# Kernel optimization log

Hardware: AMD Instinct MI355X
Metric: run time of the kernel (lower is better)

## Reference

```python
import jax, jax.numpy as jnp
import numpy as np

B, N, F = 256, 32, 256
NUM_PASSING = 2


def _fc_edges(n):
    # all ordered pairs (send -> rec), i != j, matching NRI-style encode matrices
    send, rec = [], []
    for i in range(n):
        for j in range(n):
            if i != j:
                send.append(i)
                rec.append(j)
    return np.array(send, np.int32), np.array(rec, np.int32)


def setup_inputs() -> dict:
    key = jax.random.key(0)
    ks = jax.random.split(key, 16)
    send_np, rec_np = _fc_edges(N)

    def xavier(k, shape):
        fan_in, fan_out = shape
        std = (2.0 / (fan_in + fan_out)) ** 0.5
        return jax.random.normal(k, shape, jnp.float32) * std

    bias = lambda d: jnp.full((d,), 0.1, jnp.float32)
    return {
        "x": jax.random.normal(ks[0], (B, N, F), jnp.float32),
        "rec_idx": jnp.asarray(rec_np),
        "send_idx": jnp.asarray(send_np),
        "w_in1": xavier(ks[1], (F, 256)), "b_in1": bias(256),
        "w_in2": xavier(ks[2], (256, 256)), "b_in2": bias(256),
        "w_e1": xavier(ks[3], (512, 256)), "b_e1": bias(256),
        "w_e2": xavier(ks[4], (256, 256)), "b_e2": bias(256),
        "w_n1": xavier(ks[5], (256, 256)), "b_n1": bias(256),
        "w_n2": xavier(ks[6], (256, 256)), "b_n2": bias(256),
    }


def _mlp(h, wa, ba, wb, bb):
    # Linear -> ReLU -> (Dropout p=0) -> Linear -> ReLU
    return jax.nn.relu(jax.nn.relu(h @ wa + ba) @ wb + bb)


def reference(x, rec_idx, send_idx,
              w_in1, b_in1, w_in2, b_in2,
              w_e1, b_e1, w_e2, b_e2,
              w_n1, b_n1, w_n2, b_n2):
    n_nodes = x.shape[-2]
    # in-degree per node == rec_encode.sum(0)
    deg = jax.ops.segment_sum(jnp.ones_like(rec_idx, x.dtype), rec_idx,
                              num_segments=n_nodes)  # [N]
    h = _mlp(x, w_in1, b_in1, w_in2, b_in2)  # [B, N, 256]
    for _ in range(NUM_PASSING):
        # node2edge: gather (== one-hot matmul), cat [sends, recs]
        edges = jnp.concatenate([h[:, send_idx, :], h[:, rec_idx, :]], axis=-1)  # [B, E, 512]
        e = _mlp(edges, w_e1, b_e1, w_e2, b_e2)  # [B, E, 256]
        # edge2node: scatter-sum by receiver then divide by in-degree (mean)
        e_t = jnp.swapaxes(e, 0, 1)  # [E, B, 256]
        agg = jax.ops.segment_sum(e_t, rec_idx, num_segments=n_nodes)  # [N, B, 256]
        agg = jnp.swapaxes(agg, 0, 1) / deg[None, :, None]  # [B, N, 256]
        h = _mlp(agg, w_n1, b_n1, w_n2, b_n2)
    return h
```

## Files before the change

kernel.cpp:

```cpp
#include <hip/hip_runtime.h>


typedef short bf16x8 __attribute__((ext_vector_type(8)));
typedef float f32x4 __attribute__((ext_vector_type(4)));
typedef unsigned short ushort_t;

__device__ __forceinline__ unsigned short f2bf(float f) {
    unsigned u = __float_as_uint(f);
    u += 0x7fff + ((u >> 16) & 1);
    return (unsigned short)(u >> 16);
}
__device__ __forceinline__ float lo16f(unsigned w) { return __uint_as_float(w << 16); }
__device__ __forceinline__ float hi16f(unsigned w) { return __uint_as_float(w & 0xffff0000u); }
__device__ __forceinline__ unsigned cvt_pk_bf16(float lo, float hi) {
    unsigned r;
    asm volatile("v_cvt_pk_bf16_f32 %0, %1, %2" : "=v"(r) : "v"(lo), "v"(hi));
    return r;
}
__device__ __forceinline__ void gload16(const void* g, void* l) {
    __builtin_amdgcn_global_load_lds(
        (const __attribute__((address_space(1))) void*)g,
        (__attribute__((address_space(3))) void*)l, 16, 0, 0);
}

__global__ __launch_bounds__(256) void prep_weights(
    const float* __restrict__ w_in1, const float* __restrict__ w_in2,
    const float* __restrict__ w_e1,  const float* __restrict__ w_e2,
    const float* __restrict__ w_n1,  const float* __restrict__ w_n2,
    ushort_t* __restrict__ dst)
{
    __shared__ ushort_t tile[32][264];
    const int wid = blockIdx.x >> 3;
    const int kb  = blockIdx.x & 7;
    const float* src;
    switch (wid) {
        case 0: src = w_in1; break;
        case 1: src = w_in2; break;
        case 2: src = w_e1; break;
        case 3: src = w_e1 + 65536; break;
        case 4: src = w_e2; break;
        case 5: src = w_n1; break;
        default: src = w_n2; break;
    }
    const int t = threadIdx.x;
#pragma unroll
    for (int k0 = 0; k0 < 32; k0++)
        tile[k0][t] = f2bf(src[(size_t)(kb * 32 + k0) * 256 + t]);
    __syncthreads();
    ushort_t* base = dst + wid * 65536 + kb * 8192 + t * 32;
    const int sw = (t >> 1) & 3;
#pragma unroll
    for (int kc = 0; kc < 4; kc++) {
        union { uint4 q; ushort_t u[8]; } w;
#pragma unroll
        for (int ko = 0; ko < 8; ko++) w.u[ko] = tile[kc * 8 + ko][t];
        *(uint4*)&base[(kc ^ sw) * 8] = w.q;
    }
}

__global__ __launch_bounds__(256) void conv_x(
    const float* __restrict__ x, ushort_t* __restrict__ xb, int n8)
{
    int i = blockIdx.x * 256 + threadIdx.x;
    if (i >= n8) return;
    const float4* p = (const float4*)x + (size_t)i * 2;
    float4 a = p[0], b = p[1];
    ushort4 o0 = make_ushort4(f2bf(a.x), f2bf(a.y), f2bf(a.z), f2bf(a.w));
    ushort4 o1 = make_ushort4(f2bf(b.x), f2bf(b.y), f2bf(b.z), f2bf(b.w));
    ((ushort4*)xb)[(size_t)i * 2]     = o0;
    ((ushort4*)xb)[(size_t)i * 2 + 1] = o1;
}


__device__ __forceinline__ void layer_to_lds(
    const ushort_t* __restrict__ wimg, const float* __restrict__ bias,
    const ushort_t* __restrict__ As, ushort_t* __restrict__ Ad,
    const int w, const int lr, const int lg)
{
    int boffs[4]; float4 b4[4];
#pragma unroll
    for (int fn = 0; fn < 4; fn++) {
        const int n = w * 64 + fn * 16 + lr;
        boffs[fn] = n * 32 + ((lg ^ ((n >> 1) & 3)) * 8);
        b4[fn] = *(const float4*)&bias[w * 64 + fn * 16 + lg * 4];
    }
    bf16x8 bc[4];
#pragma unroll
    for (int fn = 0; fn < 4; fn++) bc[fn] = *(const bf16x8*)&wimg[boffs[fn]];
    f32x4 acc[4][2] = {};
#pragma unroll
    for (int kb = 0; kb < 8; kb++) {
        bf16x8 bn[4];
        if (kb < 7)
#pragma unroll
            for (int fn = 0; fn < 4; fn++)
                bn[fn] = *(const bf16x8*)&wimg[(kb + 1) * 8192 + boffs[fn]];
        bf16x8 af[2];
#pragma unroll
        for (int fm = 0; fm < 2; fm++) {
            const int r = fm * 16 + lr;
            af[fm] = *(const bf16x8*)&As[r * 256 + (((kb * 4 + lg) ^ (r & 7)) * 8)];
        }
#pragma unroll
        for (int fn = 0; fn < 4; fn++)
#pragma unroll
            for (int fm = 0; fm < 2; fm++)
                acc[fn][fm] = __builtin_amdgcn_mfma_f32_16x16x32_bf16(
                    bc[fn], af[fm], acc[fn][fm], 0, 0, 0);
        if (kb < 7)
#pragma unroll
            for (int fn = 0; fn < 4; fn++) bc[fn] = bn[fn];
    }
#pragma unroll
    for (int fn = 0; fn < 4; fn++) {
        const int k0 = w * 64 + fn * 16 + lg * 4;
        const int kc = k0 >> 3, kj = k0 & 7;
#pragma unroll
        for (int fm = 0; fm < 2; fm++) {
            const int m = fm * 16 + lr;
            float v0 = fmaxf(acc[fn][fm][0] + b4[fn].x, 0.f);
            float v1 = fmaxf(acc[fn][fm][1] + b4[fn].y, 0.f);
            float v2 = fmaxf(acc[fn][fm][2] + b4[fn].z, 0.f);
            float v3 = fmaxf(acc[fn][fm][3] + b4[fn].w, 0.f);
            uint2 q = { cvt_pk_bf16(v0, v1), cvt_pk_bf16(v2, v3) };
            *(uint2*)&Ad[m * 256 + ((kc ^ (m & 7)) * 8) + kj] = q;
        }
    }
}

__device__ __forceinline__ void layer_e1(
    const ushort_t* __restrict__ wE, const float* __restrict__ bE,
    const ushort_t* __restrict__ As, ushort_t* __restrict__ UVb,
    const int m0, const int w, const int lr, const int lg)
{
    const ushort_t* wimg = (w < 2) ? wE : (wE + 65536);
    const int nb = (w & 1) * 128;
    int boffs[8]; float4 b4[8];
#pragma unroll
    for (int fn = 0; fn < 8; fn++) {
        const int n = nb + fn * 16 + lr;
        boffs[fn] = n * 32 + ((lg ^ ((n >> 1) & 3)) * 8);
        if (w < 2) b4[fn] = *(const float4*)&bE[nb + fn * 16 + lg * 4];
        else       b4[fn] = make_float4(0.f, 0.f, 0.f, 0.f);
    }
    bf16x8 bc[8];
#pragma unroll
    for (int fn = 0; fn < 8; fn++) bc[fn] = *(const bf16x8*)&wimg[boffs[fn]];
    f32x4 acc[8][2] = {};
#pragma unroll
    for (int kb = 0; kb < 8; kb++) {
        bf16x8 bn[8];
        if (kb < 7)
#pragma unroll
            for (int fn = 0; fn < 8; fn++)
                bn[fn] = *(const bf16x8*)&wimg[(kb + 1) * 8192 + boffs[fn]];
        bf16x8 af[2];
#pragma unroll
        for (int fm = 0; fm < 2; fm++) {
            const int r = fm * 16 + lr;
            af[fm] = *(const bf16x8*)&As[r * 256 + (((kb * 4 + lg) ^ (r & 7)) * 8)];
        }
#pragma unroll
        for (int fn = 0; fn < 8; fn++)
#pragma unroll
            for (int fm = 0; fm < 2; fm++)
                acc[fn][fm] = __builtin_amdgcn_mfma_f32_16x16x32_bf16(
                    bc[fn], af[fm], acc[fn][fm], 0, 0, 0);
        if (kb < 7)
#pragma unroll
            for (int fn = 0; fn < 8; fn++) bc[fn] = bn[fn];
    }
#pragma unroll
    for (int fn = 0; fn < 8; fn++) {
        const int nglob = w * 128 + fn * 16 + lg * 4;
#pragma unroll
        for (int fm = 0; fm < 2; fm++) {
            const int node = m0 + fm * 16 + lr;
            float v0 = acc[fn][fm][0] + b4[fn].x;
            float v1 = acc[fn][fm][1] + b4[fn].y;
            float v2 = acc[fn][fm][2] + b4[fn].z;
            float v3 = acc[fn][fm][3] + b4[fn].w;
            uint2 q = { cvt_pk_bf16(v0, v1), cvt_pk_bf16(v2, v3) };
            *(uint2*)&UVb[(size_t)node * 512 + nglob] = q;
        }
    }
}

__device__ __forceinline__ void layer_fin(
    const ushort_t* __restrict__ wimg, const float* __restrict__ bias,
    const ushort_t* __restrict__ As, float* __restrict__ out,
    const int m0, const int w, const int lr, const int lg)
{
    int boffs[4]; float4 b4[4];
#pragma unroll
    for (int fn = 0; fn < 4; fn++) {
        const int n = w * 64 + fn * 16 + lr;
        boffs[fn] = n * 32 + ((lg ^ ((n >> 1) & 3)) * 8);
        b4[fn] = *(const float4*)&bias[w * 64 + fn * 16 + lg * 4];
    }
    bf16x8 bc[4];
#pragma unroll
    for (int fn = 0; fn < 4; fn++) bc[fn] = *(const bf16x8*)&wimg[boffs[fn]];
    f32x4 acc[4][2] = {};
#pragma unroll
    for (int kb = 0; kb < 8; kb++) {
        bf16x8 bn[4];
        if (kb < 7)
#pragma unroll
            for (int fn = 0; fn < 4; fn++)
                bn[fn] = *(const bf16x8*)&wimg[(kb + 1) * 8192 + boffs[fn]];
        bf16x8 af[2];
#pragma unroll
        for (int fm = 0; fm < 2; fm++) {
            const int r = fm * 16 + lr;
            af[fm] = *(const bf16x8*)&As[r * 256 + (((kb * 4 + lg) ^ (r & 7)) * 8)];
        }
#pragma unroll
        for (int fn = 0; fn < 4; fn++)
#pragma unroll
            for (int fm = 0; fm < 2; fm++)
                acc[fn][fm] = __builtin_amdgcn_mfma_f32_16x16x32_bf16(
                    bc[fn], af[fm], acc[fn][fm], 0, 0, 0);
        if (kb < 7)
#pragma unroll
            for (int fn = 0; fn < 4; fn++) bc[fn] = bn[fn];
    }
#pragma unroll
    for (int fn = 0; fn < 4; fn++) {
        const int col = w * 64 + fn * 16 + lg * 4;
#pragma unroll
        for (int fm = 0; fm < 2; fm++) {
            const int row = m0 + fm * 16 + lr;
            float4 o;
            o.x = fmaxf(acc[fn][fm][0] + b4[fn].x, 0.f);
            o.y = fmaxf(acc[fn][fm][1] + b4[fn].y, 0.f);
            o.z = fmaxf(acc[fn][fm][2] + b4[fn].z, 0.f);
            o.w = fmaxf(acc[fn][fm][3] + b4[fn].w, 0.f);
            *(float4*)&out[(size_t)row * 256 + col] = o;
        }
    }
}

template <int THREE>
__global__ __launch_bounds__(256, 2) void mlp_chain(
    const ushort_t* __restrict__ in,
    const ushort_t* __restrict__ wA, const float* __restrict__ bA,
    const ushort_t* __restrict__ wB, const float* __restrict__ bB,
    const ushort_t* __restrict__ wE, const float* __restrict__ bE,
    void* __restrict__ out)
{
    __shared__ ushort_t A0[32 * 256];
    __shared__ ushort_t A1[32 * 256];
    const int m0 = blockIdx.x * 32;
    const int t = threadIdx.x;
    const int lane = t & 63, w = t >> 6;
    const int lr = lane & 15, lg = lane >> 4;

#pragma unroll
    for (int i = 0; i < 4; i++) {
        const int r = i * 8 + (t >> 5);
        const int p = t & 31;
        gload16(in + (size_t)(m0 + r) * 256 + ((p ^ (r & 7)) * 8), &A0[i * 2048 + t * 8]);
    }
    __syncthreads();

    layer_to_lds(wA, bA, A0, A1, w, lr, lg);
    __syncthreads();
    if constexpr (THREE) {
        layer_to_lds(wB, bB, A1, A0, w, lr, lg);
        __syncthreads();
        layer_e1(wE, bE, A0, (ushort_t*)out, m0, w, lr, lg);
    } else {
        layer_fin(wB, bB, A1, (float*)out, m0, w, lr, lg);
    }
}

__global__ __launch_bounds__(256, 2) void edge_fused(
    const ushort_t* __restrict__ UVb,
    const ushort_t* __restrict__ WBsw,
    const float* __restrict__ b2,
    ushort_t* __restrict__ agg)
{
    __shared__ ushort_t As[2][128 * 64];

    const int logical = (blockIdx.x & 7) * 256 + (blockIdx.x >> 3);
    const int bb = logical >> 3;
    const int g0 = (logical & 7) * 4;
    const int t = threadIdx.x;
    const int lane = t & 63;
    const int w = t >> 6;
    const int lr = lane & 15, lg = lane >> 4;

    const int brow = t >> 1;
    const int kh = t & 1;
    const int jr = brow >> 5;
    const int s = brow & 31;
    const int j = g0 + jr;
    const int si = (s == 31) ? j : (s + (s >= j ? 1 : 0));
    const ushort_t* up = UVb + (size_t)(bb * 32 + si) * 512 + kh * 32;
    const ushort_t* vp = UVb + (size_t)(bb * 32 + j) * 512 + 256 + kh * 32;
    const int rs7 = brow & 7;
    int aw[4];
#pragma unroll
    for (int i = 0; i < 4; i++)
        aw[i] = brow * 64 + (((kh * 4 + i) ^ rs7) * 8);

    const int acof0 = ((lg ^ (lr & 7)) * 8) + lr * 64;
    const int bbase = (w * 64 + lr) * 32 + ((lg ^ ((lr >> 1) & 3)) * 8);

    auto build = [&](int buf, const uint4* u, const uint4* v) {
#pragma unroll
        for (int i = 0; i < 4; i++) {
            uint4 q;
            q.x = cvt_pk_bf16(fmaxf(lo16f(u[i].x) + lo16f(v[i].x), 0.f),
                              fmaxf(hi16f(u[i].x) + hi16f(v[i].x), 0.f));
            q.y = cvt_pk_bf16(fmaxf(lo16f(u[i].y) + lo16f(v[i].y), 0.f),
                              fmaxf(hi16f(u[i].y) + hi16f(v[i].y), 0.f));
            q.z = cvt_pk_bf16(fmaxf(lo16f(u[i].z) + lo16f(v[i].z), 0.f),
                              fmaxf(hi16f(u[i].z) + hi16f(v[i].z), 0.f));
            q.w = cvt_pk_bf16(fmaxf(lo16f(u[i].w) + lo16f(v[i].w), 0.f),
                              fmaxf(hi16f(u[i].w) + hi16f(v[i].w), 0.f));
            *(uint4*)&As[buf][aw[i]] = q;
        }
    };

    {
        uint4 u[4], v[4];
#pragma unroll
        for (int i = 0; i < 4; i++) {
            u[i] = *(const uint4*)(up + i * 8);
            v[i] = *(const uint4*)(vp + i * 8);
        }
        build(0, u, v);
    }
    bf16x8 bc[2][4];
#pragma unroll
    for (int ks = 0; ks < 2; ks++)
#pragma unroll
        for (int fn = 0; fn < 4; fn++)
            bc[ks][fn] = *(const bf16x8*)&WBsw[ks * 8192 + bbase + fn * 512];

    f32x4 acc[8][4] = {};

#pragma unroll
    for (int kb = 0; kb < 4; kb++) {
        __syncthreads();
        uint4 u[4], v[4];
        if (kb < 3) {
            const ushort_t* upn = up + (kb + 1) * 64;
            const ushort_t* vpn = vp + (kb + 1) * 64;
#pragma unroll
            for (int i = 0; i < 4; i++) {
                u[i] = *(const uint4*)(upn + i * 8);
                v[i] = *(const uint4*)(vpn + i * 8);
            }
        }
        __builtin_amdgcn_s_setprio(1);
#pragma unroll
        for (int ks = 0; ks < 2; ks++) {
            bf16x8 af[8];
#pragma unroll
            for (int m = 0; m < 8; m++)
                af[m] = *(const bf16x8*)&As[kb & 1][m * 1024 + (acof0 ^ (ks * 32))];
#pragma unroll
            for (int fn = 0; fn < 4; fn++)
#pragma unroll
                for (int m = 0; m < 8; m++)
                    acc[m][fn] = __builtin_amdgcn_mfma_f32_16x16x32_bf16(
                        af[m], bc[ks][fn], acc[m][fn], 0, 0, 0);
        }
        __builtin_amdgcn_s_setprio(0);
        if (kb < 3) {
#pragma unroll
            for (int ks = 0; ks < 2; ks++)
#pragma unroll
                for (int fn = 0; fn < 4; fn++)
                    bc[ks][fn] = *(const bf16x8*)&WBsw[((kb + 1) * 2 + ks) * 8192
                                                       + bbase + fn * 512];
            build((kb + 1) & 1, u, v);
        }
    }

#pragma unroll
    for (int fn = 0; fn < 4; fn++) {
        const int col = w * 64 + fn * 16 + lr;
        const float bvf = b2[col];
#pragma unroll
        for (int recv = 0; recv < 4; recv++) {
            float sum = 0.f;
#pragma unroll
            for (int q = 0; q < 2; q++) {
                const int fm = recv * 2 + q;
#pragma unroll
                for (int r = 0; r < 4; r++) {
                    float v = fmaxf(acc[fm][fn][r] + bvf, 0.f);
                    if (!(q == 1 && lg == 3 && r == 3)) sum += v;
                }
            }
            sum += __shfl_xor(sum, 16);
            sum += __shfl_xor(sum, 32);
            if (lane < 16)
                agg[(size_t)(bb * 32 + g0 + recv) * 256 + col] = f2bf(sum * (1.0f / 31.0f));
        }
    }
}

extern "C" void kernel_launch(void* const* d_in, const int* in_sizes, int n_in,
                              void* d_out, int out_size, void* d_ws, size_t ws_size,
                              hipStream_t stream)
{
    const float* x     = (const float*)d_in[0];
    const float* w_in1 = (const float*)d_in[3];
    const float* b_in1 = (const float*)d_in[4];
    const float* w_in2 = (const float*)d_in[5];
    const float* b_in2 = (const float*)d_in[6];
    const float* w_e1  = (const float*)d_in[7];
    const float* b_e1  = (const float*)d_in[8];
    const float* w_e2  = (const float*)d_in[9];
    const float* b_e2  = (const float*)d_in[10];
    const float* w_n1  = (const float*)d_in[11];
    const float* b_n1  = (const float*)d_in[12];
    const float* w_n2  = (const float*)d_in[13];
    const float* b_n2  = (const float*)d_in[14];

    char* ws = (char*)d_ws;
    size_t off = 0;
    auto alloc = [&](size_t n) { char* p = ws + off; off += (n + 255) & ~(size_t)255; return p; };

    ushort_t* wt  = (ushort_t*)alloc(7 * 65536 * sizeof(ushort_t));
    ushort_t* xb  = (ushort_t*)alloc(8192 * 256 * 2);
    ushort_t* UVb = (ushort_t*)alloc(8192 * 512 * 2);
    ushort_t* ag  = (ushort_t*)alloc(8192 * 256 * 2);
    (void)ws_size; (void)in_sizes; (void)n_in; (void)out_size;

    prep_weights<<<56, 256, 0, stream>>>(w_in1, w_in2, w_e1, w_e2, w_n1, w_n2, wt);
    conv_x<<<1024, 256, 0, stream>>>(x, xb, 262144);

    mlp_chain<1><<<256, 256, 0, stream>>>(xb,
        wt + 0 * 65536, b_in1, wt + 1 * 65536, b_in2, wt + 2 * 65536, b_e1, UVb);
    edge_fused<<<2048, 256, 0, stream>>>(UVb, wt + 4 * 65536, b_e2, ag);
    mlp_chain<1><<<256, 256, 0, stream>>>(ag,
        wt + 5 * 65536, b_n1, wt + 6 * 65536, b_n2, wt + 2 * 65536, b_e1, UVb);
    edge_fused<<<2048, 256, 0, stream>>>(UVb, wt + 4 * 65536, b_e2, ag);
    mlp_chain<0><<<256, 256, 0, stream>>>(ag,
        wt + 5 * 65536, b_n1, wt + 6 * 65536, b_n2, nullptr, nullptr, d_out);
}
```

Before: 134.2 us.

## Split edge kernel over output columns, widen MLP blocks, merge prep kernels

The edge kernel now splits each unit's 256 output columns into two halves, giving 4096 blocks. It stages the W_e2 weight tiles into LDS with async global-to-LDS loads, double-buffered, and uses a 2x2 warp tiling instead of per-warp register-held weights. The MLP chain kernels move to 512 threads so each warp computes fewer output columns. Weight conversion and input conversion are merged into one launch. The aim is more parallelism and occupancy plus one fewer launch, at the cost of rebuilding the gathered A tile twice per unit and more LDS use per block.

```diff
diff --git a/kernel.cpp b/kernel.cpp
--- a/kernel.cpp
+++ b/kernel.cpp
@@ -23,13 +23,25 @@
         (__attribute__((address_space(3))) void*)l, 16, 0, 0);
 }
 
-__global__ __launch_bounds__(256) void prep_weights(
+__global__ __launch_bounds__(256) void prep_all(
     const float* __restrict__ w_in1, const float* __restrict__ w_in2,
     const float* __restrict__ w_e1,  const float* __restrict__ w_e2,
     const float* __restrict__ w_n1,  const float* __restrict__ w_n2,
-    ushort_t* __restrict__ dst)
+    ushort_t* __restrict__ dst,
+    const float* __restrict__ x, ushort_t* __restrict__ xb)
 {
     __shared__ ushort_t tile[32][264];
+    const int t = threadIdx.x;
+    if (blockIdx.x >= 56) {
+        const int i = (blockIdx.x - 56) * 256 + t;
+        const float4* p = (const float4*)x + (size_t)i * 2;
+        float4 a = p[0], b = p[1];
+        ushort4 o0 = make_ushort4(f2bf(a.x), f2bf(a.y), f2bf(a.z), f2bf(a.w));
+        ushort4 o1 = make_ushort4(f2bf(b.x), f2bf(b.y), f2bf(b.z), f2bf(b.w));
+        ((ushort4*)xb)[(size_t)i * 2]     = o0;
+        ((ushort4*)xb)[(size_t)i * 2 + 1] = o1;
+        return;
+    }
     const int wid = blockIdx.x >> 3;
     const int kb  = blockIdx.x & 7;
     const float* src;
@@ -42,7 +54,6 @@
         case 5: src = w_n1; break;
         default: src = w_n2; break;
     }
-    const int t = threadIdx.x;
 #pragma unroll
     for (int k0 = 0; k0 < 32; k0++)
         tile[k0][t] = f2bf(src[(size_t)(kb * 32 + k0) * 256 + t]);
@@ -58,42 +69,29 @@
     }
 }
 
-__global__ __launch_bounds__(256) void conv_x(
-    const float* __restrict__ x, ushort_t* __restrict__ xb, int n8)
-{
-    int i = blockIdx.x * 256 + threadIdx.x;
-    if (i >= n8) return;
-    const float4* p = (const float4*)x + (size_t)i * 2;
-    float4 a = p[0], b = p[1];
-    ushort4 o0 = make_ushort4(f2bf(a.x), f2bf(a.y), f2bf(a.z), f2bf(a.w));
-    ushort4 o1 = make_ushort4(f2bf(b.x), f2bf(b.y), f2bf(b.z), f2bf(b.w));
-    ((ushort4*)xb)[(size_t)i * 2]     = o0;
-    ((ushort4*)xb)[(size_t)i * 2 + 1] = o1;
-}
-
 
 __device__ __forceinline__ void layer_to_lds(
     const ushort_t* __restrict__ wimg, const float* __restrict__ bias,
     const ushort_t* __restrict__ As, ushort_t* __restrict__ Ad,
     const int w, const int lr, const int lg)
 {
-    int boffs[4]; float4 b4[4];
-#pragma unroll
-    for (int fn = 0; fn < 4; fn++) {
-        const int n = w * 64 + fn * 16 + lr;
-        boffs[fn] = n * 32 + ((lg ^ ((n >> 1) & 3)) * 8);
-        b4[fn] = *(const float4*)&bias[w * 64 + fn * 16 + lg * 4];
-    }
-    bf16x8 bc[4];
-#pragma unroll
-    for (int fn = 0; fn < 4; fn++) bc[fn] = *(const bf16x8*)&wimg[boffs[fn]];
-    f32x4 acc[4][2] = {};
+    int boffs[2]; float4 b4[2];
+#pragma unroll
+    for (int fn = 0; fn < 2; fn++) {
+        const int n = w * 32 + fn * 16 + lr;
+        boffs[fn] = n * 32 + ((lg ^ ((lr >> 1) & 3)) * 8);
+        b4[fn] = *(const float4*)&bias[w * 32 + fn * 16 + lg * 4];
+    }
+    bf16x8 bc[2];
+#pragma unroll
+    for (int fn = 0; fn < 2; fn++) bc[fn] = *(const bf16x8*)&wimg[boffs[fn]];
+    f32x4 acc[2][2] = {};
 #pragma unroll
     for (int kb = 0; kb < 8; kb++) {
-        bf16x8 bn[4];
-        if (kb < 7)
-#pragma unroll
-            for (int fn = 0; fn < 4; fn++)
+        bf16x8 bn[2];
+        if (kb < 7)
+#pragma unroll
+            for (int fn = 0; fn < 2; fn++)
                 bn[fn] = *(const bf16x8*)&wimg[(kb + 1) * 8192 + boffs[fn]];
         bf16x8 af[2];
 #pragma unroll
@@ -102,18 +100,18 @@
             af[fm] = *(const bf16x8*)&As[r * 256 + (((kb * 4 + lg) ^ (r & 7)) * 8)];
         }
 #pragma unroll
-        for (int fn = 0; fn < 4; fn++)
+        for (int fn = 0; fn < 2; fn++)
 #pragma unroll
             for (int fm = 0; fm < 2; fm++)
                 acc[fn][fm] = __builtin_amdgcn_mfma_f32_16x16x32_bf16(
                     bc[fn], af[fm], acc[fn][fm], 0, 0, 0);
         if (kb < 7)
 #pragma unroll
-            for (int fn = 0; fn < 4; fn++) bc[fn] = bn[fn];
-    }
-#pragma unroll
-    for (int fn = 0; fn < 4; fn++) {
-        const int k0 = w * 64 + fn * 16 + lg * 4;
+            for (int fn = 0; fn < 2; fn++) bc[fn] = bn[fn];
+    }
+#pragma unroll
+    for (int fn = 0; fn < 2; fn++) {
+        const int k0 = w * 32 + fn * 16 + lg * 4;
         const int kc = k0 >> 3, kj = k0 & 7;
 #pragma unroll
         for (int fm = 0; fm < 2; fm++) {
@@ -133,26 +131,26 @@
     const ushort_t* __restrict__ As, ushort_t* __restrict__ UVb,
     const int m0, const int w, const int lr, const int lg)
 {
-    const ushort_t* wimg = (w < 2) ? wE : (wE + 65536);
-    const int nb = (w & 1) * 128;
-    int boffs[8]; float4 b4[8];
-#pragma unroll
-    for (int fn = 0; fn < 8; fn++) {
+    const ushort_t* wimg = (w < 4) ? wE : (wE + 65536);
+    const int nb = (w & 3) * 64;
+    int boffs[4]; float4 b4[4];
+#pragma unroll
+    for (int fn = 0; fn < 4; fn++) {
         const int n = nb + fn * 16 + lr;
-        boffs[fn] = n * 32 + ((lg ^ ((n >> 1) & 3)) * 8);
-        if (w < 2) b4[fn] = *(const float4*)&bE[nb + fn * 16 + lg * 4];
+        boffs[fn] = n * 32 + ((lg ^ ((lr >> 1) & 3)) * 8);
+        if (w < 4) b4[fn] = *(const float4*)&bE[nb + fn * 16 + lg * 4];
         else       b4[fn] = make_float4(0.f, 0.f, 0.f, 0.f);
     }
-    bf16x8 bc[8];
-#pragma unroll
-    for (int fn = 0; fn < 8; fn++) bc[fn] = *(const bf16x8*)&wimg[boffs[fn]];
-    f32x4 acc[8][2] = {};
+    bf16x8 bc[4];
+#pragma unroll
+    for (int fn = 0; fn < 4; fn++) bc[fn] = *(const bf16x8*)&wimg[boffs[fn]];
+    f32x4 acc[4][2] = {};
 #pragma unroll
     for (int kb = 0; kb < 8; kb++) {
-        bf16x8 bn[8];
-        if (kb < 7)
-#pragma unroll
-            for (int fn = 0; fn < 8; fn++)
+        bf16x8 bn[4];
+        if (kb < 7)
+#pragma unroll
+            for (int fn = 0; fn < 4; fn++)
                 bn[fn] = *(const bf16x8*)&wimg[(kb + 1) * 8192 + boffs[fn]];
         bf16x8 af[2];
 #pragma unroll
@@ -161,18 +159,18 @@
             af[fm] = *(const bf16x8*)&As[r * 256 + (((kb * 4 + lg) ^ (r & 7)) * 8)];
         }
 #pragma unroll
-        for (int fn = 0; fn < 8; fn++)
+        for (int fn = 0; fn < 4; fn++)
 #pragma unroll
             for (int fm = 0; fm < 2; fm++)
                 acc[fn][fm] = __builtin_amdgcn_mfma_f32_16x16x32_bf16(
                     bc[fn], af[fm], acc[fn][fm], 0, 0, 0);
         if (kb < 7)
 #pragma unroll
-            for (int fn = 0; fn < 8; fn++) bc[fn] = bn[fn];
-    }
-#pragma unroll
-    for (int fn = 0; fn < 8; fn++) {
-        const int nglob = w * 128 + fn * 16 + lg * 4;
+            for (int fn = 0; fn < 4; fn++) bc[fn] = bn[fn];
+    }
+#pragma unroll
+    for (int fn = 0; fn < 4; fn++) {
+        const int nglob = w * 64 + fn * 16 + lg * 4;
 #pragma unroll
         for (int fm = 0; fm < 2; fm++) {
             const int node = m0 + fm * 16 + lr;
@@ -191,23 +189,23 @@
     const ushort_t* __restrict__ As, float* __restrict__ out,
     const int m0, const int w, const int lr, const int lg)
 {
-    int boffs[4]; float4 b4[4];
-#pragma unroll
-    for (int fn = 0; fn < 4; fn++) {
-        const int n = w * 64 + fn * 16 + lr;
-        boffs[fn] = n * 32 + ((lg ^ ((n >> 1) & 3)) * 8);
-        b4[fn] = *(const float4*)&bias[w * 64 + fn * 16 + lg * 4];
-    }
-    bf16x8 bc[4];
-#pragma unroll
-    for (int fn = 0; fn < 4; fn++) bc[fn] = *(const bf16x8*)&wimg[boffs[fn]];
-    f32x4 acc[4][2] = {};
+    int boffs[2]; float4 b4[2];
+#pragma unroll
+    for (int fn = 0; fn < 2; fn++) {
+        const int n = w * 32 + fn * 16 + lr;
+        boffs[fn] = n * 32 + ((lg ^ ((lr >> 1) & 3)) * 8);
+        b4[fn] = *(const float4*)&bias[w * 32 + fn * 16 + lg * 4];
+    }
+    bf16x8 bc[2];
+#pragma unroll
+    for (int fn = 0; fn < 2; fn++) bc[fn] = *(const bf16x8*)&wimg[boffs[fn]];
+    f32x4 acc[2][2] = {};
 #pragma unroll
     for (int kb = 0; kb < 8; kb++) {
-        bf16x8 bn[4];
-        if (kb < 7)
-#pragma unroll
-            for (int fn = 0; fn < 4; fn++)
+        bf16x8 bn[2];
+        if (kb < 7)
+#pragma unroll
+            for (int fn = 0; fn < 2; fn++)
                 bn[fn] = *(const bf16x8*)&wimg[(kb + 1) * 8192 + boffs[fn]];
         bf16x8 af[2];
 #pragma unroll
@@ -216,18 +214,18 @@
             af[fm] = *(const bf16x8*)&As[r * 256 + (((kb * 4 + lg) ^ (r & 7)) * 8)];
         }
 #pragma unroll
-        for (int fn = 0; fn < 4; fn++)
+        for (int fn = 0; fn < 2; fn++)
 #pragma unroll
             for (int fm = 0; fm < 2; fm++)
                 acc[fn][fm] = __builtin_amdgcn_mfma_f32_16x16x32_bf16(
                     bc[fn], af[fm], acc[fn][fm], 0, 0, 0);
         if (kb < 7)
 #pragma unroll
-            for (int fn = 0; fn < 4; fn++) bc[fn] = bn[fn];
-    }
-#pragma unroll
-    for (int fn = 0; fn < 4; fn++) {
-        const int col = w * 64 + fn * 16 + lg * 4;
+            for (int fn = 0; fn < 2; fn++) bc[fn] = bn[fn];
+    }
+#pragma unroll
+    for (int fn = 0; fn < 2; fn++) {
+        const int col = w * 32 + fn * 16 + lg * 4;
 #pragma unroll
         for (int fm = 0; fm < 2; fm++) {
             const int row = m0 + fm * 16 + lr;
@@ -242,7 +240,7 @@
 }
 
 template <int THREE>
-__global__ __launch_bounds__(256, 2) void mlp_chain(
+__global__ __launch_bounds__(512, 2) void mlp_chain(
     const ushort_t* __restrict__ in,
     const ushort_t* __restrict__ wA, const float* __restrict__ bA,
     const ushort_t* __restrict__ wB, const float* __restrict__ bB,
@@ -256,11 +254,11 @@
     const int lane = t & 63, w = t >> 6;
     const int lr = lane & 15, lg = lane >> 4;
 
-#pragma unroll
-    for (int i = 0; i < 4; i++) {
-        const int r = i * 8 + (t >> 5);
-        const int p = t & 31;
-        gload16(in + (size_t)(m0 + r) * 256 + ((p ^ (r & 7)) * 8), &A0[i * 2048 + t * 8]);
+    {
+        const int r0 = t >> 5, p0 = t & 31;
+        gload16(in + (size_t)(m0 + r0) * 256 + ((p0 ^ (r0 & 7)) * 8), &A0[t * 8]);
+        const int r1 = r0 + 16;
+        gload16(in + (size_t)(m0 + r1) * 256 + ((p0 ^ (r1 & 7)) * 8), &A0[(t + 512) * 8]);
     }
     __syncthreads();
 
@@ -275,20 +273,24 @@
     }
 }
 
-__global__ __launch_bounds__(256, 2) void edge_fused(
+__global__ __launch_bounds__(256, 3) void edge_fused(
     const ushort_t* __restrict__ UVb,
     const ushort_t* __restrict__ WBsw,
     const float* __restrict__ b2,
     ushort_t* __restrict__ agg)
 {
     __shared__ ushort_t As[2][128 * 64];
-
-    const int logical = (blockIdx.x & 7) * 256 + (blockIdx.x >> 3);
-    const int bb = logical >> 3;
-    const int g0 = (logical & 7) * 4;
+    __shared__ ushort_t Bs[2][128 * 64];
+
+    const int logical = (blockIdx.x & 7) * 512 + (blockIdx.x >> 3);
+    const int unit = logical >> 1;
+    const int n0 = (logical & 1) * 128;
+    const int bb = unit >> 3;
+    const int g0 = (unit & 7) * 4;
     const int t = threadIdx.x;
     const int lane = t & 63;
     const int w = t >> 6;
+    const int wm = w >> 1, wn = w & 1;
     const int lr = lane & 15, lg = lane >> 4;
 
     const int brow = t >> 1;
@@ -305,8 +307,13 @@
     for (int i = 0; i < 4; i++)
         aw[i] = brow * 64 + (((kh * 4 + i) ^ rs7) * 8);
 
-    const int acof0 = ((lg ^ (lr & 7)) * 8) + lr * 64;
-    const int bbase = (w * 64 + lr) * 32 + ((lg ^ ((lr >> 1) & 3)) * 8);
+    int aoff[4];
+#pragma unroll
+    for (int f = 0; f < 4; f++) {
+        const int r = wm * 64 + f * 16 + lr;
+        aoff[f] = r * 64 + ((lg ^ (r & 7)) * 8);
+    }
+    const int bfbase = (wn * 64 + lr) * 32 + ((lg ^ ((lr >> 1) & 3)) * 8);
 
     auto build = [&](int buf, const uint4* u, const uint4* v) {
 #pragma unroll
@@ -323,7 +330,14 @@
             *(uint4*)&As[buf][aw[i]] = q;
         }
     };
-
+    auto stageB = [&](int kb2, int buf) {
+        const ushort_t* src = WBsw + kb2 * 8192 + n0 * 32 + t * 8;
+#pragma unroll
+        for (int q = 0; q < 4; q++)
+            gload16(src + q * 2048 + (q >= 2 ? 4096 : 0), &Bs[buf][q * 2048 + t * 8]);
+    };
+
+    stageB(0, 0);
     {
         uint4 u[4], v[4];
 #pragma unroll
@@ -333,20 +347,16 @@
         }
         build(0, u, v);
     }
-    bf16x8 bc[2][4];
-#pragma unroll
-    for (int ks = 0; ks < 2; ks++)
-#pragma unroll
-        for (int fn = 0; fn < 4; fn++)
-            bc[ks][fn] = *(const bf16x8*)&WBsw[ks * 8192 + bbase + fn * 512];
-
-    f32x4 acc[8][4] = {};
+
+    f32x4 acc[4][4] = {};
 
 #pragma unroll
     for (int kb = 0; kb < 4; kb++) {
+        const int cur = kb & 1;
         __syncthreads();
         uint4 u[4], v[4];
         if (kb < 3) {
+            stageB((kb + 1) * 2, cur ^ 1);
             const ushort_t* upn = up + (kb + 1) * 64;
             const ushort_t* vpn = vp + (kb + 1) * 64;
 #pragma unroll
@@ -358,49 +368,44 @@
         __builtin_amdgcn_s_setprio(1);
 #pragma unroll
         for (int ks = 0; ks < 2; ks++) {
-            bf16x8 af[8];
-#pragma unroll
-            for (int m = 0; m < 8; m++)
-                af[m] = *(const bf16x8*)&As[kb & 1][m * 1024 + (acof0 ^ (ks * 32))];
-#pragma unroll
-            for (int fn = 0; fn < 4; fn++)
-#pragma unroll
-                for (int m = 0; m < 8; m++)
+            bf16x8 af[4];
+#pragma unroll
+            for (int m = 0; m < 4; m++)
+                af[m] = *(const bf16x8*)&As[cur][aoff[m] ^ (ks * 32)];
+#pragma unroll
+            for (int fn = 0; fn < 4; fn++) {
+                bf16x8 bf = *(const bf16x8*)&Bs[cur][ks * 4096 + bfbase + fn * 512];
+#pragma unroll
+                for (int m = 0; m < 4; m++)
                     acc[m][fn] = __builtin_amdgcn_mfma_f32_16x16x32_bf16(
-                        af[m], bc[ks][fn], acc[m][fn], 0, 0, 0);
+                        af[m], bf, acc[m][fn], 0, 0, 0);
+            }
         }
         __builtin_amdgcn_s_setprio(0);
-        if (kb < 3) {
-#pragma unroll
-            for (int ks = 0; ks < 2; ks++)
-#pragma unroll
-                for (int fn = 0; fn < 4; fn++)
-                    bc[ks][fn] = *(const bf16x8*)&WBsw[((kb + 1) * 2 + ks) * 8192
-                                                       + bbase + fn * 512];
-            build((kb + 1) & 1, u, v);
-        }
+        if (kb < 3) build(cur ^ 1, u, v);
     }
 
 #pragma unroll
     for (int fn = 0; fn < 4; fn++) {
-        const int col = w * 64 + fn * 16 + lr;
+        const int col = n0 + wn * 64 + fn * 16 + lr;
         const float bvf = b2[col];
 #pragma unroll
-        for (int recv = 0; recv < 4; recv++) {
+        for (int h = 0; h < 2; h++) {
             float sum = 0.f;
 #pragma unroll
             for (int q = 0; q < 2; q++) {
-                const int fm = recv * 2 + q;
+                const int f = 2 * h + q;
 #pragma unroll
                 for (int r = 0; r < 4; r++) {
-                    float v = fmaxf(acc[fm][fn][r] + bvf, 0.f);
+                    float v = fmaxf(acc[f][fn][r] + bvf, 0.f);
                     if (!(q == 1 && lg == 3 && r == 3)) sum += v;
                 }
             }
             sum += __shfl_xor(sum, 16);
             sum += __shfl_xor(sum, 32);
             if (lane < 16)
-                agg[(size_t)(bb * 32 + g0 + recv) * 256 + col] = f2bf(sum * (1.0f / 31.0f));
+                agg[(size_t)(bb * 32 + g0 + wm * 2 + h) * 256 + col] =
+                    f2bf(sum * (1.0f / 31.0f));
         }
     }
 }
@@ -433,15 +438,14 @@
     ushort_t* ag  = (ushort_t*)alloc(8192 * 256 * 2);
     (void)ws_size; (void)in_sizes; (void)n_in; (void)out_size;
 
-    prep_weights<<<56, 256, 0, stream>>>(w_in1, w_in2, w_e1, w_e2, w_n1, w_n2, wt);
-    conv_x<<<1024, 256, 0, stream>>>(x, xb, 262144);
-
-    mlp_chain<1><<<256, 256, 0, stream>>>(xb,
+    prep_all<<<1080, 256, 0, stream>>>(w_in1, w_in2, w_e1, w_e2, w_n1, w_n2, wt, x, xb);
+
+    mlp_chain<1><<<256, 512, 0, stream>>>(xb,
         wt + 0 * 65536, b_in1, wt + 1 * 65536, b_in2, wt + 2 * 65536, b_e1, UVb);
-    edge_fused<<<2048, 256, 0, stream>>>(UVb, wt + 4 * 65536, b_e2, ag);
-    mlp_chain<1><<<256, 256, 0, stream>>>(ag,
+    edge_fused<<<4096, 256, 0, stream>>>(UVb, wt + 4 * 65536, b_e2, ag);
+    mlp_chain<1><<<256, 512, 0, stream>>>(ag,
         wt + 5 * 65536, b_n1, wt + 6 * 65536, b_n2, wt + 2 * 65536, b_e1, UVb);
-    edge_fused<<<2048, 256, 0, stream>>>(UVb, wt + 4 * 65536, b_e2, ag);
-    mlp_chain<0><<<256, 256, 0, stream>>>(ag,
+    edge_fused<<<4096, 256, 0, stream>>>(UVb, wt + 4 * 65536, b_e2, ag);
+    mlp_chain<0><<<256, 512, 0, stream>>>(ag,
         wt + 5 * 65536, b_n1, wt + 6 * 65536, b_n2, nullptr, nullptr, d_out);
 }
```

Result: slower. 178.5 us (+33.0%).

## Split edge kernel output columns across blocks, use 2x2 warp tiling, merge prep kernels

Applied to the files above, without the earlier changes.

The edge kernel now covers half of the 256 output columns per block, launching twice as many blocks. Each warp takes a 64x64 tile in a 2x2 arrangement instead of 128 rows by 64 columns, which halves the accumulators and allows 3 blocks per CU. The A tile is still built by every block, so the gather and build work for the edge inputs is doubled. The syncthreads is swapped for a lighter barrier that waits only on LDS counters, and the weight-prep and x-conversion kernels are merged into one launch to save a launch.

```diff
diff --git a/kernel.cpp b/kernel.cpp
--- a/kernel.cpp
+++ b/kernel.cpp
@@ -22,14 +22,31 @@
         (const __attribute__((address_space(1))) void*)g,
         (__attribute__((address_space(3))) void*)l, 16, 0, 0);
 }
-
-__global__ __launch_bounds__(256) void prep_weights(
+__device__ __forceinline__ void soft_barrier() {
+    asm volatile("s_waitcnt lgkmcnt(0)" ::: "memory");
+    __builtin_amdgcn_sched_barrier(0);
+    __builtin_amdgcn_s_barrier();
+}
+
+__global__ __launch_bounds__(256) void prep_all(
     const float* __restrict__ w_in1, const float* __restrict__ w_in2,
     const float* __restrict__ w_e1,  const float* __restrict__ w_e2,
     const float* __restrict__ w_n1,  const float* __restrict__ w_n2,
-    ushort_t* __restrict__ dst)
+    ushort_t* __restrict__ dst,
+    const float* __restrict__ x, ushort_t* __restrict__ xb)
 {
     __shared__ ushort_t tile[32][264];
+    const int t = threadIdx.x;
+    if (blockIdx.x >= 56) {
+        const int i = (blockIdx.x - 56) * 256 + t;
+        const float4* p = (const float4*)x + (size_t)i * 2;
+        float4 a = p[0], b = p[1];
+        ushort4 o0 = make_ushort4(f2bf(a.x), f2bf(a.y), f2bf(a.z), f2bf(a.w));
+        ushort4 o1 = make_ushort4(f2bf(b.x), f2bf(b.y), f2bf(b.z), f2bf(b.w));
+        ((ushort4*)xb)[(size_t)i * 2]     = o0;
+        ((ushort4*)xb)[(size_t)i * 2 + 1] = o1;
+        return;
+    }
     const int wid = blockIdx.x >> 3;
     const int kb  = blockIdx.x & 7;
     const float* src;
@@ -42,7 +59,6 @@
         case 5: src = w_n1; break;
         default: src = w_n2; break;
     }
-    const int t = threadIdx.x;
 #pragma unroll
     for (int k0 = 0; k0 < 32; k0++)
         tile[k0][t] = f2bf(src[(size_t)(kb * 32 + k0) * 256 + t]);
@@ -56,19 +72,6 @@
         for (int ko = 0; ko < 8; ko++) w.u[ko] = tile[kc * 8 + ko][t];
         *(uint4*)&base[(kc ^ sw) * 8] = w.q;
     }
-}
-
-__global__ __launch_bounds__(256) void conv_x(
-    const float* __restrict__ x, ushort_t* __restrict__ xb, int n8)
-{
-    int i = blockIdx.x * 256 + threadIdx.x;
-    if (i >= n8) return;
-    const float4* p = (const float4*)x + (size_t)i * 2;
-    float4 a = p[0], b = p[1];
-    ushort4 o0 = make_ushort4(f2bf(a.x), f2bf(a.y), f2bf(a.z), f2bf(a.w));
-    ushort4 o1 = make_ushort4(f2bf(b.x), f2bf(b.y), f2bf(b.z), f2bf(b.w));
-    ((ushort4*)xb)[(size_t)i * 2]     = o0;
-    ((ushort4*)xb)[(size_t)i * 2 + 1] = o1;
 }
 
 
@@ -275,7 +278,7 @@
     }
 }
 
-__global__ __launch_bounds__(256, 2) void edge_fused(
+__global__ __launch_bounds__(256, 3) void edge_fused(
     const ushort_t* __restrict__ UVb,
     const ushort_t* __restrict__ WBsw,
     const float* __restrict__ b2,
@@ -283,12 +286,15 @@
 {
     __shared__ ushort_t As[2][128 * 64];
 
-    const int logical = (blockIdx.x & 7) * 256 + (blockIdx.x >> 3);
-    const int bb = logical >> 3;
-    const int g0 = (logical & 7) * 4;
+    const int logical = (blockIdx.x & 7) * 512 + (blockIdx.x >> 3);
+    const int unit = logical >> 1;
+    const int nh = logical & 1;
+    const int bb = unit >> 3;
+    const int g0 = (unit & 7) * 4;
     const int t = threadIdx.x;
     const int lane = t & 63;
     const int w = t >> 6;
+    const int wm = w >> 1, wn = w & 1;
     const int lr = lane & 15, lg = lane >> 4;
 
     const int brow = t >> 1;
@@ -305,8 +311,18 @@
     for (int i = 0; i < 4; i++)
         aw[i] = brow * 64 + (((kh * 4 + i) ^ rs7) * 8);
 
-    const int acof0 = ((lg ^ (lr & 7)) * 8) + lr * 64;
-    const int bbase = (w * 64 + lr) * 32 + ((lg ^ ((lr >> 1) & 3)) * 8);
+    int aoff[4];
+#pragma unroll
+    for (int f = 0; f < 4; f++) {
+        const int r = wm * 64 + f * 16 + lr;
+        aoff[f] = r * 64 + ((lg ^ (r & 7)) * 8);
+    }
+    int boff[4];
+#pragma unroll
+    for (int fn = 0; fn < 4; fn++) {
+        const int n = nh * 128 + wn * 64 + fn * 16 + lr;
+        boff[fn] = n * 32 + ((lg ^ ((n >> 1) & 3)) * 8);
+    }
 
     auto build = [&](int buf, const uint4* u, const uint4* v) {
 #pragma unroll
@@ -338,13 +354,14 @@
     for (int ks = 0; ks < 2; ks++)
 #pragma unroll
         for (int fn = 0; fn < 4; fn++)
-            bc[ks][fn] = *(const bf16x8*)&WBsw[ks * 8192 + bbase + fn * 512];
-
-    f32x4 acc[8][4] = {};
+            bc[ks][fn] = *(const bf16x8*)&WBsw[ks * 8192 + boff[fn]];
+
+    f32x4 acc[4][4] = {};
 
 #pragma unroll
     for (int kb = 0; kb < 4; kb++) {
-        __syncthreads();
+        const int cur = kb & 1;
+        soft_barrier();
         uint4 u[4], v[4];
         if (kb < 3) {
             const ushort_t* upn = up + (kb + 1) * 64;
@@ -358,14 +375,14 @@
         __builtin_amdgcn_s_setprio(1);
 #pragma unroll
         for (int ks = 0; ks < 2; ks++) {
-            bf16x8 af[8];
-#pragma unroll
-            for (int m = 0; m < 8; m++)
-                af[m] = *(const bf16x8*)&As[kb & 1][m * 1024 + (acof0 ^ (ks * 32))];
+            bf16x8 af[4];
+#pragma unroll
+            for (int m = 0; m < 4; m++)
+                af[m] = *(const bf16x8*)&As[cur][aoff[m] ^ (ks * 32)];
 #pragma unroll
             for (int fn = 0; fn < 4; fn++)
 #pragma unroll
-                for (int m = 0; m < 8; m++)
+                for (int m = 0; m < 4; m++)
                     acc[m][fn] = __builtin_amdgcn_mfma_f32_16x16x32_bf16(
                         af[m], bc[ks][fn], acc[m][fn], 0, 0, 0);
         }
@@ -376,31 +393,32 @@
 #pragma unroll
                 for (int fn = 0; fn < 4; fn++)
                     bc[ks][fn] = *(const bf16x8*)&WBsw[((kb + 1) * 2 + ks) * 8192
-                                                       + bbase + fn * 512];
-            build((kb + 1) & 1, u, v);
-        }
-    }
-
-#pragma unroll
-    for (int fn = 0; fn < 4; fn++) {
-        const int col = w * 64 + fn * 16 + lr;
+                                                       + boff[fn]];
+            build(cur ^ 1, u, v);
+        }
+    }
+
+#pragma unroll
+    for (int fn = 0; fn < 4; fn++) {
+        const int col = nh * 128 + wn * 64 + fn * 16 + lr;
         const float bvf = b2[col];
 #pragma unroll
-        for (int recv = 0; recv < 4; recv++) {
+        for (int h = 0; h < 2; h++) {
             float sum = 0.f;
 #pragma unroll
             for (int q = 0; q < 2; q++) {
-                const int fm = recv * 2 + q;
+                const int f = 2 * h + q;
 #pragma unroll
                 for (int r = 0; r < 4; r++) {
-                    float v = fmaxf(acc[fm][fn][r] + bvf, 0.f);
+                    float v = fmaxf(acc[f][fn][r] + bvf, 0.f);
                     if (!(q == 1 && lg == 3 && r == 3)) sum += v;
                 }
             }
             sum += __shfl_xor(sum, 16);
             sum += __shfl_xor(sum, 32);
             if (lane < 16)
-                agg[(size_t)(bb * 32 + g0 + recv) * 256 + col] = f2bf(sum * (1.0f / 31.0f));
+                agg[(size_t)(bb * 32 + g0 + wm * 2 + h) * 256 + col] =
+                    f2bf(sum * (1.0f / 31.0f));
         }
     }
 }
@@ -433,15 +451,14 @@
     ushort_t* ag  = (ushort_t*)alloc(8192 * 256 * 2);
     (void)ws_size; (void)in_sizes; (void)n_in; (void)out_size;
 
-    prep_weights<<<56, 256, 0, stream>>>(w_in1, w_in2, w_e1, w_e2, w_n1, w_n2, wt);
-    conv_x<<<1024, 256, 0, stream>>>(x, xb, 262144);
+    prep_all<<<1080, 256, 0, stream>>>(w_in1, w_in2, w_e1, w_e2, w_n1, w_n2, wt, x, xb);
 
     mlp_chain<1><<<256, 256, 0, stream>>>(xb,
         wt + 0 * 65536, b_in1, wt + 1 * 65536, b_in2, wt + 2 * 65536, b_e1, UVb);
-    edge_fused<<<2048, 256, 0, stream>>>(UVb, wt + 4 * 65536, b_e2, ag);
+    edge_fused<<<4096, 256, 0, stream>>>(UVb, wt + 4 * 65536, b_e2, ag);
     mlp_chain<1><<<256, 256, 0, stream>>>(ag,
         wt + 5 * 65536, b_n1, wt + 6 * 65536, b_n2, wt + 2 * 65536, b_e1, UVb);
-    edge_fused<<<2048, 256, 0, stream>>>(UVb, wt + 4 * 65536, b_e2, ag);
+    edge_fused<<<4096, 256, 0, stream>>>(UVb, wt + 4 * 65536, b_e2, ag);
     mlp_chain<0><<<256, 256, 0, stream>>>(ag,
         wt + 5 * 65536, b_n1, wt + 6 * 65536, b_n2, nullptr, nullptr, d_out);
 }
```

New measurement: 146.2 us. 9.0% more time.
